# Performance work log

Measured on AMD Instinct MI355X. Metric: run time of the kernel, lower is better.

The kernel has to match this reference:

```python
import jax, jax.numpy as jnp
import numpy as np

NUM_EXPERTS = 8
EMBED_DIM = 1024
EXPERT_DIM = 2048
TOP_K = 2
B, T = 2, 1024


def setup_inputs() -> dict:
    key = jax.random.key(0)
    ks = jax.random.split(key, 7)
    std = 0.02
    return {
        "x": jax.random.normal(ks[0], (B, T, EMBED_DIM), dtype=jnp.float32),
        "gate_inputs": jax.random.normal(ks[1], (B, T, EMBED_DIM), dtype=jnp.float32),
        "gate_kernel": jax.random.normal(ks[2], (EMBED_DIM, NUM_EXPERTS), dtype=jnp.float32) * std,
        "per_expert_scale": jnp.ones((NUM_EXPERTS,), dtype=jnp.float32),
        "gate_proj_w": jax.random.normal(ks[3], (NUM_EXPERTS, EMBED_DIM, EXPERT_DIM), dtype=jnp.float32) * std,
        "up_proj_w": jax.random.normal(ks[4], (NUM_EXPERTS, EMBED_DIM, EXPERT_DIM), dtype=jnp.float32) * std,
        "down_proj_w": jax.random.normal(ks[5], (NUM_EXPERTS, EXPERT_DIM, EMBED_DIM), dtype=jnp.float32) * std,
    }


def reference(x, gate_inputs, gate_kernel, per_expert_scale,
              gate_proj_w, up_proj_w, down_proj_w):
    Bb, Tt, D = x.shape
    x_flat = x.reshape(Bb * Tt, D)          # [t, e]
    g_flat = gate_inputs.reshape(Bb * Tt, D)

    logits = jnp.dot(g_flat, gate_kernel)   # [t, n]
    topk_logits, topk_idx = jax.lax.top_k(logits, TOP_K)  # [t, k]
    weights = jax.nn.sigmoid(topk_logits)   # [t, k]

    # Dense all-expert projections (as in the original module)
    gate_out = jnp.einsum('te,ned->tnd', x_flat, gate_proj_w)  # [t, n, d]
    up_out = jnp.einsum('te,ned->tnd', x_flat, up_proj_w)
    act = jax.nn.gelu(gate_out) * up_out
    expert_out = jnp.einsum('tnd,nde->tne', act, down_proj_w)  # [t, n, e]
    expert_out = expert_out * per_expert_scale[None, :, None]

    mask = jax.nn.one_hot(topk_idx, NUM_EXPERTS, dtype=expert_out.dtype)  # [t, k, n]
    selected = jnp.einsum('tkn,tne->tke', mask, expert_out)               # [t, k, e]
    out = jnp.einsum('tk,tke->te', weights, selected)                     # [t, e]
    return out.reshape(Bb, Tt, D)
```

## Files before the change

kernel.cpp:

```cpp
#include <hip/hip_runtime.h>
#include <math.h>
#include <stdint.h>

#define NE 8
#define ED 1024
#define FD 2048
#define NTOK 2048
#define BM 128
#define BN 128
#define BK 64

typedef unsigned short u16;
typedef unsigned int u32;
typedef __attribute__((ext_vector_type(4))) float f32x4;
typedef __attribute__((ext_vector_type(8))) short s16x8;
typedef __attribute__((ext_vector_type(4))) unsigned int u32v4;


__device__ __forceinline__ u16 f2bf(float f) {
    u32 u = __builtin_bit_cast(u32, f);
    u32 r = u + 0x7fffu + ((u >> 16) & 1u);
    return (u16)(r >> 16);
}

typedef __attribute__((address_space(1))) const void gvoid_t;
typedef __attribute__((address_space(3))) void lvoid_t;

__device__ __forceinline__ void gload16(const void* g, void* l) {
    __builtin_amdgcn_global_load_lds((gvoid_t*)g, (lvoid_t*)l, 16, 0, 0);
}


#define WS_CNT 0u
#define WS_OFF 64u
#define WS_TOK 256u
#define WS_WT  65792u
#define WS_XB  131328u
#define WS_WG  (8u << 20)
#define WS_WU  41943040u
#define WS_WD  75497472u
#define WS_ACT 109051904u
#define WS_NEED 130023424u


__global__ __launch_bounds__(256) void k_router(
        const float* __restrict__ gin, const float* __restrict__ gk,
        int* __restrict__ cnt, int* __restrict__ tok, float* __restrict__ wl) {
    int lane = threadIdx.x & 63;
    int t = (blockIdx.x * 256 + threadIdx.x) >> 6;
    if (t >= NTOK) return;
    const float* row = gin + (size_t)t * ED;
    float acc[NE];
#pragma unroll
    for (int e = 0; e < NE; e++) acc[e] = 0.f;
    for (int i = lane; i < ED; i += 64) {
        float v = row[i];
        const float* g = gk + i * NE;
#pragma unroll
        for (int e = 0; e < NE; e++) acc[e] = fmaf(v, g[e], acc[e]);
    }
#pragma unroll
    for (int e = 0; e < NE; e++) {
#pragma unroll
        for (int off = 32; off > 0; off >>= 1)
            acc[e] += __shfl_down(acc[e], off, 64);
    }
    if (lane == 0) {
        int b0 = 0; float v0 = acc[0];
#pragma unroll
        for (int e = 1; e < NE; e++) if (acc[e] > v0) { v0 = acc[e]; b0 = e; }
        int b1 = -1; float v1 = -3.4e38f;
#pragma unroll
        for (int e = 0; e < NE; e++) if (e != b0 && acc[e] > v1) { v1 = acc[e]; b1 = e; }
        float w0 = 1.f / (1.f + __expf(-v0));
        float w1 = 1.f / (1.f + __expf(-v1));
        int p0 = atomicAdd(&cnt[b0], 1);
        tok[b0 * NTOK + p0] = t; wl[b0 * NTOK + p0] = w0;
        int p1 = atomicAdd(&cnt[b1], 1);
        tok[b1 * NTOK + p1] = t; wl[b1 * NTOK + p1] = w1;
    }
}

__global__ void k_scan(const int* __restrict__ cnt, int* __restrict__ off) {
    if (threadIdx.x == 0 && blockIdx.x == 0) {
        int a = 0;
#pragma unroll
        for (int e = 0; e < NE; e++) { off[e] = a; a += (cnt[e] + 127) & ~127; }
        off[NE] = a;
    }
}


__global__ __launch_bounds__(256) void k_cvtx(const float4* __restrict__ x, uint2* __restrict__ xb) {
    int i = blockIdx.x * 256 + threadIdx.x;
    float4 v = x[i];
    uint2 o;
    o.x = (u32)f2bf(v.x) | ((u32)f2bf(v.y) << 16);
    o.y = (u32)f2bf(v.z) | ((u32)f2bf(v.w) << 16);
    xb[i] = o;
}


__global__ __launch_bounds__(256) void k_cvtw(
        const float* __restrict__ wgf, const float* __restrict__ wuf, const float* __restrict__ wdf,
        u16* __restrict__ og, u16* __restrict__ ou, u16* __restrict__ od) {
    int b = blockIdx.x;
    const float* src; u16* dst; int NT, KC, ROW; int bi = b;
    if (b < 2048)      { src = wgf; dst = og; NT = 16; KC = 16; ROW = FD; }
    else if (b < 4096) { bi = b - 2048; src = wuf; dst = ou; NT = 16; KC = 16; ROW = FD; }
    else               { bi = b - 4096; src = wdf; dst = od; NT = 8;  KC = 32; ROW = ED; }
    int kc = bi % KC; int r = bi / KC; int nt = r % NT; int e = r / NT;
    const float* base = src + (size_t)e * (size_t)(KC * 64) * ROW + (size_t)kc * 64 * ROW + nt * 128;
    u16* ob = dst + (size_t)bi * 8192;

    __shared__ u32 sl[32 * 132];
    int tid = threadIdx.x;

    {
        int nq = (tid & 31) * 4;
        int kph = tid >> 5;
#pragma unroll
        for (int jj = 0; jj < 4; jj++) {
            int kp = kph * 4 + jj;
            const float* rp0 = base + (size_t)(2 * kp) * ROW + nq;
            float4 f0 = *(const float4*)rp0;
            float4 f1 = *(const float4*)(rp0 + ROW);
            u32v4 w;
            w.x = (u32)f2bf(f0.x) | ((u32)f2bf(f1.x) << 16);
            w.y = (u32)f2bf(f0.y) | ((u32)f2bf(f1.y) << 16);
            w.z = (u32)f2bf(f0.z) | ((u32)f2bf(f1.z) << 16);
            w.w = (u32)f2bf(f0.w) | ((u32)f2bf(f1.w) << 16);
            *(u32v4*)(sl + kp * 132 + nq) = w;
        }
    }
    __syncthreads();

#pragma unroll
    for (int jg = 0; jg < 4; jg++) {
        int v = jg * 256 + tid;
        int n = v >> 3, p = v & 7;
        int lg = p ^ (n & 7);
        u32v4 w;
        w.x = sl[(lg * 4 + 0) * 132 + n];
        w.y = sl[(lg * 4 + 1) * 132 + n];
        w.z = sl[(lg * 4 + 2) * 132 + n];
        w.w = sl[(lg * 4 + 3) * 132 + n];
        *(u32v4*)(ob + (size_t)n * 64 + p * 8) = w;
    }
}


__global__ __launch_bounds__(256, 2) void k_passA(
        const u16* __restrict__ xb, const u16* __restrict__ wg, const u16* __restrict__ wu,
        const int* __restrict__ cnt, const int* __restrict__ off,
        const int* __restrict__ tok, u16* __restrict__ act) {
    int e = blockIdx.z, mt = blockIdx.y, nt = blockIdx.x;
    int c = cnt[e];
    if (mt * BM >= c) return;
    int rmax = c - mt * BM; if (rmax > BM) rmax = BM;

    __shared__ u16 sA[BM * BK];
    __shared__ u16 sBg[BN * BK];
    __shared__ u16 sBu[BN * BK];

    int tid = threadIdx.x;
    int lane = tid & 63, wv = tid >> 6;
    int wm = wv >> 1, wn = wv & 1;
    int col = lane & 15, quad = lane >> 4;
    int swz = col & 7;

    f32x4 zero = {0.f, 0.f, 0.f, 0.f};
    f32x4 ag[4][4], au[4][4];
#pragma unroll
    for (int i = 0; i < 4; i++)
#pragma unroll
        for (int j = 0; j < 4; j++) { ag[i][j] = zero; au[i][j] = zero; }

    int am = tid >> 1, ah = tid & 1;
    int ridx = mt * BM + am; if (ridx > c - 1) ridx = c - 1;
    int trow = tok[e * NTOK + ridx];
    const u16* asrc = xb + (size_t)trow * ED + ah * 32;
    u16* adst = sA + am * BK;

    const u16* gg = wg + ((size_t)(e * 16 + nt) * 16) * 8192;
    const u16* gu = wu + ((size_t)(e * 16 + nt) * 16) * 8192;
    const u16* bsrc0 = (wv < 2 ? gg : gu);
    int bhalf = (wv & 1) * 4096;
    u16* bdst = (wv < 2 ? sBg : sBu) + bhalf;

    for (int kc = 0; kc < 16; kc++) {
        __syncthreads();
        const u16* bs = bsrc0 + (size_t)kc * 8192 + bhalf + lane * 8;
#pragma unroll
        for (int i = 0; i < 8; i++)
            gload16(bs + i * 512, bdst + i * 512);
        const u16* as = asrc + kc * 64;
#pragma unroll
        for (int j = 0; j < 4; j++) {
            int pg = (ah * 4 + j) ^ (am & 7);
            *(u32v4*)(adst + pg * 8) = *(const u32v4*)(as + j * 8);
        }
        __syncthreads();
#pragma unroll
        for (int st = 0; st < 2; st++) {
            int poff = ((st * 4 + quad) ^ swz) * 8;
            s16x8 af[4];
#pragma unroll
            for (int mf = 0; mf < 4; mf++)
                af[mf] = *(const s16x8*)(sA + (wm * 64 + mf * 16 + col) * BK + poff);
#pragma unroll
            for (int nf = 0; nf < 4; nf++) {
                int brow = (wn * 64 + nf * 16 + col) * BK + poff;
                s16x8 bg = *(const s16x8*)(sBg + brow);
                s16x8 bu = *(const s16x8*)(sBu + brow);
#pragma unroll
                for (int mf = 0; mf < 4; mf++) {
                    ag[mf][nf] = __builtin_amdgcn_mfma_f32_16x16x32_bf16(af[mf], bg, ag[mf][nf], 0, 0, 0);
                    au[mf][nf] = __builtin_amdgcn_mfma_f32_16x16x32_bf16(af[mf], bu, au[mf][nf], 0, 0, 0);
                }
            }
        }
    }

    int tile = (off[e] >> 7) + mt;
    u16* ab = act + (size_t)tile * (32 * 8192);
#pragma unroll
    for (int mf = 0; mf < 4; mf++) {
#pragma unroll
        for (int reg = 0; reg < 4; reg++) {
            int m = wm * 64 + mf * 16 + quad * 4 + reg;
            if (m < rmax) {
#pragma unroll
                for (int nf = 0; nf < 4; nf++) {
                    float gv = ag[mf][nf][reg];
                    float uv = au[mf][nf][reg];
                    float z = 0.7978845608028654f * (gv + 0.044715f * gv * gv * gv);
                    float ez = __expf(-2.f * fabsf(z));
                    float th = (1.f - ez) / (1.f + ez);
                    th = (z < 0.f) ? -th : th;
                    float a = 0.5f * gv * (1.f + th) * uv;
                    int ng = nt * 128 + wn * 64 + nf * 16 + col;
                    int pos = ((((ng >> 3) & 7) ^ (m & 7)) * 8) | (ng & 7);
                    ab[(size_t)(ng >> 6) * 8192 + (size_t)m * 64 + pos] = f2bf(a);
                }
            }
        }
    }
}


__global__ __launch_bounds__(256, 3) void k_passB(
        const u16* __restrict__ act, const u16* __restrict__ wd,
        const int* __restrict__ cnt, const int* __restrict__ off,
        const int* __restrict__ tok, const float* __restrict__ wl,
        const float* __restrict__ scale, float* __restrict__ out) {
    int e = blockIdx.z, mt = blockIdx.y, nt = blockIdx.x;
    int c = cnt[e];
    if (mt * BM >= c) return;
    int rmax = c - mt * BM; if (rmax > BM) rmax = BM;

    __shared__ u16 sA[BM * BK];
    __shared__ u16 sB[BN * BK];

    int tid = threadIdx.x;
    int lane = tid & 63, wv = tid >> 6;
    int wm = wv >> 1, wn = wv & 1;
    int col = lane & 15, quad = lane >> 4;
    int swz = col & 7;

    f32x4 zero = {0.f, 0.f, 0.f, 0.f};
    f32x4 acc[4][4];
#pragma unroll
    for (int i = 0; i < 4; i++)
#pragma unroll
        for (int j = 0; j < 4; j++) acc[i][j] = zero;

    int tile = (off[e] >> 7) + mt;
    const u16* ga = act + (size_t)tile * (32 * 8192);
    const u16* gb = wd + ((size_t)(e * 8 + nt) * 32) * 8192;
    const u16* src0 = (wv < 2 ? ga : gb);
    int shalf = (wv & 1) * 4096;
    u16* dst0 = (wv < 2 ? sA : sB) + shalf;

    for (int kc = 0; kc < 32; kc++) {
        __syncthreads();
        const u16* s = src0 + (size_t)kc * 8192 + shalf + lane * 8;
#pragma unroll
        for (int i = 0; i < 8; i++)
            gload16(s + i * 512, dst0 + i * 512);
        __syncthreads();
#pragma unroll
        for (int st = 0; st < 2; st++) {
            int poff = ((st * 4 + quad) ^ swz) * 8;
            s16x8 af[4];
#pragma unroll
            for (int mf = 0; mf < 4; mf++)
                af[mf] = *(const s16x8*)(sA + (wm * 64 + mf * 16 + col) * BK + poff);
#pragma unroll
            for (int nf = 0; nf < 4; nf++) {
                int brow = (wn * 64 + nf * 16 + col) * BK + poff;
                s16x8 bf = *(const s16x8*)(sB + brow);
#pragma unroll
                for (int mf = 0; mf < 4; mf++)
                    acc[mf][nf] = __builtin_amdgcn_mfma_f32_16x16x32_bf16(af[mf], bf, acc[mf][nf], 0, 0, 0);
            }
        }
    }

    float sc = scale[e];
    int lbase = e * NTOK + mt * BM;
#pragma unroll
    for (int mf = 0; mf < 4; mf++) {
#pragma unroll
        for (int reg = 0; reg < 4; reg++) {
            int m = wm * 64 + mf * 16 + quad * 4 + reg;
            if (m < rmax) {
                int t = tok[lbase + m];
                float w = wl[lbase + m] * sc;
                float* orow = out + (size_t)t * ED + nt * 128 + wn * 64 + col;
#pragma unroll
                for (int nf = 0; nf < 4; nf++)
                    atomicAdd(orow + nf * 16, acc[mf][nf][reg] * w);
            }
        }
    }
}


extern "C" void kernel_launch(void* const* d_in, const int* in_sizes, int n_in,
                              void* d_out, int out_size, void* d_ws, size_t ws_size,
                              hipStream_t stream) {
    const float* x   = (const float*)d_in[0];
    const float* gin = (const float*)d_in[1];
    const float* gk  = (const float*)d_in[2];
    const float* sc  = (const float*)d_in[3];
    const float* wgf = (const float*)d_in[4];
    const float* wuf = (const float*)d_in[5];
    const float* wdf = (const float*)d_in[6];
    float* out = (float*)d_out;

    if (ws_size < (size_t)WS_NEED) {
        hipMemsetAsync(d_out, 0, (size_t)out_size * sizeof(float), stream);
        return;
    }

    char* ws = (char*)d_ws;
    int*   cnt = (int*)(ws + WS_CNT);
    int*   off = (int*)(ws + WS_OFF);
    int*   tok = (int*)(ws + WS_TOK);
    float* wl  = (float*)(ws + WS_WT);
    u16*   xb  = (u16*)(ws + WS_XB);
    u16*   og  = (u16*)(ws + WS_WG);
    u16*   ou  = (u16*)(ws + WS_WU);
    u16*   od  = (u16*)(ws + WS_WD);
    u16*   act = (u16*)(ws + WS_ACT);

    hipMemsetAsync(cnt, 0, 64, stream);
    hipMemsetAsync(d_out, 0, (size_t)out_size * sizeof(float), stream);

    k_router<<<dim3(512), dim3(256), 0, stream>>>(gin, gk, cnt, tok, wl);
    k_scan<<<dim3(1), dim3(64), 0, stream>>>(cnt, off);
    k_cvtx<<<dim3(2048), dim3(256), 0, stream>>>((const float4*)x, (uint2*)xb);
    k_cvtw<<<dim3(6144), dim3(256), 0, stream>>>(wgf, wuf, wdf, og, ou, od);
    k_passA<<<dim3(16, 16, NE), dim3(256), 0, stream>>>(xb, og, ou, cnt, off, tok, act);
    k_passB<<<dim3(8, 16, NE), dim3(256), 0, stream>>>(act, od, cnt, off, tok, wl, sc, out);
}
```

Measured before the change: 412.1 us.

## Switch bf16 weight/activation tiles to k-group-major layout and stream full weight rows

The weight conversion kernel now processes whole rows, 8 k-rows by the full N width, per block. Its global reads become long contiguous streams instead of 128-column patches. The packed tile layout changes from row-major-with-XOR-swizzle to k-group-major (8 groups of 128 rows by 8 bf16). passA and passB fragment loads and the activation store are updated to match this layout. The aim is cheaper fp32-to-bf16 weight conversion, which dominates memory traffic. The trade-off is that the unswizzled LDS fragment reads may see different bank-conflict behaviour.

Result: slower. 429.2 us (+4.1%).

```diff
diff --git a/kernel.cpp b/kernel.cpp
--- a/kernel.cpp
+++ b/kernel.cpp
@@ -101,51 +101,51 @@
 }
 
 
-__global__ __launch_bounds__(256) void k_cvtw(
+__global__ __launch_bounds__(256, 4) void k_cvtw(
         const float* __restrict__ wgf, const float* __restrict__ wuf, const float* __restrict__ wdf,
         u16* __restrict__ og, u16* __restrict__ ou, u16* __restrict__ od) {
     int b = blockIdx.x;
-    const float* src; u16* dst; int NT, KC, ROW; int bi = b;
-    if (b < 2048)      { src = wgf; dst = og; NT = 16; KC = 16; ROW = FD; }
-    else if (b < 4096) { bi = b - 2048; src = wuf; dst = ou; NT = 16; KC = 16; ROW = FD; }
-    else               { bi = b - 4096; src = wdf; dst = od; NT = 8;  KC = 32; ROW = ED; }
-    int kc = bi % KC; int r = bi / KC; int nt = r % NT; int e = r / NT;
-    const float* base = src + (size_t)e * (size_t)(KC * 64) * ROW + (size_t)kc * 64 * ROW + nt * 128;
-    u16* ob = dst + (size_t)bi * 8192;
-
-    __shared__ u32 sl[32 * 132];
+    const float* src; u16* dst; int ROW; int e, s;
+    if (b < 1024)      { src = wgf; dst = og; ROW = FD; e = b >> 7;  s = b & 127; }
+    else if (b < 2048) { int b2 = b - 1024; src = wuf; dst = ou; ROW = FD; e = b2 >> 7; s = b2 & 127; }
+    else               { int b2 = b - 2048; src = wdf; dst = od; ROW = ED; e = b2 >> 8; s = b2 & 255; }
+    int kc = s >> 3, g = s & 7;
+    int rpe = (ROW == FD) ? ED : FD;
+    const float* base = src + (size_t)e * (size_t)rpe * ROW + (size_t)s * 8 * ROW;
+
+    __shared__ u32 sl[4 * 2052];
     int tid = threadIdx.x;
-
-    {
-        int nq = (tid & 31) * 4;
-        int kph = tid >> 5;
-#pragma unroll
-        for (int jj = 0; jj < 4; jj++) {
-            int kp = kph * 4 + jj;
-            const float* rp0 = base + (size_t)(2 * kp) * ROW + nq;
-            float4 f0 = *(const float4*)rp0;
-            float4 f1 = *(const float4*)(rp0 + ROW);
+    int chunks = ROW >> 10;
+
+    for (int kp = 0; kp < 4; kp++) {
+        const float* r0 = base + (size_t)(2 * kp) * ROW;
+        for (int ch = 0; ch < chunks; ch++) {
+            int n4 = ch * 256 + tid;
+            float4 f0 = *((const float4*)r0 + n4);
+            float4 f1 = *((const float4*)(r0 + ROW) + n4);
             u32v4 w;
             w.x = (u32)f2bf(f0.x) | ((u32)f2bf(f1.x) << 16);
             w.y = (u32)f2bf(f0.y) | ((u32)f2bf(f1.y) << 16);
             w.z = (u32)f2bf(f0.z) | ((u32)f2bf(f1.z) << 16);
             w.w = (u32)f2bf(f0.w) | ((u32)f2bf(f1.w) << 16);
-            *(u32v4*)(sl + kp * 132 + nq) = w;
+            *(u32v4*)(sl + kp * 2052 + 4 * n4) = w;
         }
     }
     __syncthreads();
 
-#pragma unroll
-    for (int jg = 0; jg < 4; jg++) {
-        int v = jg * 256 + tid;
-        int n = v >> 3, p = v & 7;
-        int lg = p ^ (n & 7);
+    int iters = ROW >> 8;
+    for (int it = 0; it < iters; it++) {
+        int n = it * 256 + tid;
         u32v4 w;
-        w.x = sl[(lg * 4 + 0) * 132 + n];
-        w.y = sl[(lg * 4 + 1) * 132 + n];
-        w.z = sl[(lg * 4 + 2) * 132 + n];
-        w.w = sl[(lg * 4 + 3) * 132 + n];
-        *(u32v4*)(ob + (size_t)n * 64 + p * 8) = w;
+        w.x = sl[0 * 2052 + n];
+        w.y = sl[1 * 2052 + n];
+        w.z = sl[2 * 2052 + n];
+        w.w = sl[3 * 2052 + n];
+        int nt = n >> 7;
+        int img = (ROW == FD) ? ((e * 16 + nt) * 16 + kc)
+                              : ((e * 8 + nt) * 32 + kc);
+        u16* ob = dst + (size_t)img * 8192 + (size_t)g * 1024 + (size_t)(n & 127) * 8;
+        *(u32v4*)ob = w;
     }
 }
 
@@ -203,16 +203,17 @@
         __syncthreads();
 #pragma unroll
         for (int st = 0; st < 2; st++) {
-            int poff = ((st * 4 + quad) ^ swz) * 8;
+            int g4 = st * 4 + quad;
+            int aoff = (g4 ^ swz) * 8;
             s16x8 af[4];
 #pragma unroll
             for (int mf = 0; mf < 4; mf++)
-                af[mf] = *(const s16x8*)(sA + (wm * 64 + mf * 16 + col) * BK + poff);
+                af[mf] = *(const s16x8*)(sA + (wm * 64 + mf * 16 + col) * BK + aoff);
 #pragma unroll
             for (int nf = 0; nf < 4; nf++) {
-                int brow = (wn * 64 + nf * 16 + col) * BK + poff;
-                s16x8 bg = *(const s16x8*)(sBg + brow);
-                s16x8 bu = *(const s16x8*)(sBu + brow);
+                int boff = g4 * 1024 + (wn * 64 + nf * 16 + col) * 8;
+                s16x8 bg = *(const s16x8*)(sBg + boff);
+                s16x8 bu = *(const s16x8*)(sBu + boff);
 #pragma unroll
                 for (int mf = 0; mf < 4; mf++) {
                     ag[mf][nf] = __builtin_amdgcn_mfma_f32_16x16x32_bf16(af[mf], bg, ag[mf][nf], 0, 0, 0);
@@ -240,8 +241,8 @@
                     th = (z < 0.f) ? -th : th;
                     float a = 0.5f * gv * (1.f + th) * uv;
                     int ng = nt * 128 + wn * 64 + nf * 16 + col;
-                    int pos = ((((ng >> 3) & 7) ^ (m & 7)) * 8) | (ng & 7);
-                    ab[(size_t)(ng >> 6) * 8192 + (size_t)m * 64 + pos] = f2bf(a);
+                    ab[(size_t)(ng >> 6) * 8192 + (size_t)((ng >> 3) & 7) * 1024
+                       + (size_t)m * 8 + (ng & 7)] = f2bf(a);
                 }
             }
         }
@@ -266,7 +267,6 @@
     int lane = tid & 63, wv = tid >> 6;
     int wm = wv >> 1, wn = wv & 1;
     int col = lane & 15, quad = lane >> 4;
-    int swz = col & 7;
 
     f32x4 zero = {0.f, 0.f, 0.f, 0.f};
     f32x4 acc[4][4];
@@ -291,15 +291,15 @@
         __syncthreads();
 #pragma unroll
         for (int st = 0; st < 2; st++) {
-            int poff = ((st * 4 + quad) ^ swz) * 8;
+            int g4 = st * 4 + quad;
+            int abase = g4 * 1024;
             s16x8 af[4];
 #pragma unroll
             for (int mf = 0; mf < 4; mf++)
-                af[mf] = *(const s16x8*)(sA + (wm * 64 + mf * 16 + col) * BK + poff);
+                af[mf] = *(const s16x8*)(sA + abase + (wm * 64 + mf * 16 + col) * 8);
 #pragma unroll
             for (int nf = 0; nf < 4; nf++) {
-                int brow = (wn * 64 + nf * 16 + col) * BK + poff;
-                s16x8 bf = *(const s16x8*)(sB + brow);
+                s16x8 bf = *(const s16x8*)(sB + abase + (wn * 64 + nf * 16 + col) * 8);
 #pragma unroll
                 for (int mf = 0; mf < 4; mf++)
                     acc[mf][nf] = __builtin_amdgcn_mfma_f32_16x16x32_bf16(af[mf], bf, acc[mf][nf], 0, 0, 0);
@@ -361,7 +361,7 @@
     k_router<<<dim3(512), dim3(256), 0, stream>>>(gin, gk, cnt, tok, wl);
     k_scan<<<dim3(1), dim3(64), 0, stream>>>(cnt, off);
     k_cvtx<<<dim3(2048), dim3(256), 0, stream>>>((const float4*)x, (uint2*)xb);
-    k_cvtw<<<dim3(6144), dim3(256), 0, stream>>>(wgf, wuf, wdf, og, ou, od);
+    k_cvtw<<<dim3(4096), dim3(256), 0, stream>>>(wgf, wuf, wdf, og, ou, od);
     k_passA<<<dim3(16, 16, NE), dim3(256), 0, stream>>>(xb, og, ou, cnt, off, tok, act);
     k_passB<<<dim3(8, 16, NE), dim3(256), 0, stream>>>(act, od, cnt, off, tok, wl, sc, out);
 }
```
